# Optimization experiments

Hardware: AMD Instinct MI355X
Metric: run time of the kernel (lower is better)

Reference implementation:

```python
import jax, jax.numpy as jnp
import numpy as np

HEADS = 8
DIM_HEAD = 64
QUERY_DIM = 512
INNER = HEADS * DIM_HEAD
DIAG_OFFSET = 1
T_TEMP = 1.0
NEG_INF = -1e9  # used via -inf below; kept for clarity


def setup_inputs() -> dict:
    key = jax.random.key(0)
    ks = jax.random.split(key, 8)
    b, s, f = 2, 2048, 16
    x = jax.random.normal(ks[0], (b, s, f, QUERY_DIM), dtype=jnp.float32)
    pos_bias = jax.random.normal(ks[1], (HEADS, f, f), dtype=jnp.float32)
    w_scale = 0.02
    Wq = jax.random.normal(ks[2], (QUERY_DIM, INNER), dtype=jnp.float32) * w_scale
    Wk = jax.random.normal(ks[3], (QUERY_DIM, INNER), dtype=jnp.float32) * w_scale
    Wv = jax.random.normal(ks[4], (QUERY_DIM, INNER), dtype=jnp.float32) * w_scale
    Wo = jax.random.normal(ks[5], (INNER, QUERY_DIM), dtype=jnp.float32) * w_scale
    bo = jax.random.normal(ks[6], (QUERY_DIM,), dtype=jnp.float32) * w_scale
    return {"x": x, "pos_bias": pos_bias, "Wq": Wq, "Wk": Wk, "Wv": Wv, "Wo": Wo, "bo": bo}


def reference(x, pos_bias, Wq, Wk, Wv, Wo, bo):
    # x: [b, s, f, c] -- temporal attention over the frame axis f per spatial token
    b, s, f, _ = x.shape
    scale = DIM_HEAD ** -0.5
    q = (x @ Wq).reshape(b, s, f, HEADS, DIM_HEAD)
    k = (x @ Wk).reshape(b, s, f, HEADS, DIM_HEAD)
    v = (x @ Wv).reshape(b, s, f, HEADS, DIM_HEAD)
    # scores over frames: [b, s, h, f_q, f_k]
    w = jnp.einsum('bsihd,bsjhd->bshij', q * scale, k)
    w = w + pos_bias[None, None]  # [h, f, f] relative position bias
    # attend_prev_only causal mask (strict, diag_offset=1)
    causal = jnp.triu(jnp.ones((f, f), dtype=jnp.float32), k=DIAG_OFFSET)
    w = w + jnp.where(causal == 1.0, -jnp.inf, 0.0)
    # faithful to source: subtract row max, then softmax with temperature
    w = w - jax.lax.stop_gradient(jnp.max(w, axis=-1, keepdims=True))
    p = jax.nn.softmax(w.astype(jnp.float32) / T_TEMP, axis=-1).astype(w.dtype)
    out = jnp.einsum('bshij,bsjhd->bsihd', p, v).reshape(b, s, f, INNER)
    return out @ Wo + bo
```

## Files before the change

kernel.cpp:

```cpp
#include <hip/hip_runtime.h>

typedef unsigned short u16;
typedef __attribute__((ext_vector_type(8))) unsigned short u16x8;
typedef __attribute__((ext_vector_type(8))) __bf16 bf16x8;
typedef __attribute__((ext_vector_type(4))) float f32x4;

#define M_ROWS 65536
#define KDIM   512
#define NKT    8

typedef __attribute__((address_space(1))) const void gconst_void;
typedef __attribute__((address_space(3))) void lds_void;

static __device__ __forceinline__ u16 f2bf(float f) {
  unsigned u = __builtin_bit_cast(unsigned, f);
  u += 0x7FFFu + ((u >> 16) & 1u);
  return (u16)(u >> 16);
}

static __device__ __forceinline__ f32x4 mfma_bf16(u16x8 a, u16x8 b, f32x4 c) {
  return __builtin_amdgcn_mfma_f32_16x16x32_bf16(
      __builtin_bit_cast(bf16x8, a), __builtin_bit_cast(bf16x8, b), c, 0, 0, 0);
}

__global__ void conv_x(const float* __restrict__ x, u16* __restrict__ xb) {
  const size_t t = (size_t)blockIdx.x * 256 + threadIdx.x;
  f32x4 a = *(const f32x4*)(x + t * 8);
  f32x4 b = *(const f32x4*)(x + t * 8 + 4);
  u16x8 w;
#pragma unroll
  for (int e = 0; e < 4; ++e) { w[e] = f2bf(a[e]); w[e + 4] = f2bf(b[e]); }
  *(u16x8*)(xb + t * 8) = w;
}

__global__ void convW_qkv_t(const float* __restrict__ Wq, const float* __restrict__ Wk,
                            const float* __restrict__ Wv, u16* __restrict__ Wt) {
  __shared__ float tile[32][33];
  const int bn = blockIdx.x * 32;
  const int bk = blockIdx.y * 32;
  const int tx = threadIdx.x & 31, ty = threadIdx.x >> 5;
  const float* W = (bn < 512) ? Wq : ((bn < 1024) ? Wk : Wv);
  const int coln = bn & 511;
#pragma unroll
  for (int r = 0; r < 32; r += 8)
    tile[ty + r][tx] = W[(size_t)(bk + ty + r) * 512 + coln + tx];
  __syncthreads();
#pragma unroll
  for (int r = 0; r < 32; r += 8)
    Wt[(size_t)(bn + ty + r) * 512 + bk + tx] = f2bf(tile[tx][ty + r]);
}

__global__ void convWo_t(const float* __restrict__ Wo, u16* __restrict__ Wt) {
  __shared__ float tile[32][33];
  const int bn = blockIdx.x * 32;
  const int bk = blockIdx.y * 32;
  const int tx = threadIdx.x & 31, ty = threadIdx.x >> 5;
#pragma unroll
  for (int r = 0; r < 32; r += 8)
    tile[ty + r][tx] = Wo[(size_t)(bk + ty + r) * 512 + bn + tx];
  __syncthreads();
#pragma unroll
  for (int r = 0; r < 32; r += 8)
    Wt[(size_t)(bn + ty + r) * 512 + bk + tx] = f2bf(tile[tx][ty + r]);
}

__global__ __launch_bounds__(512, 2)
void gemm_qkv_attn(const u16* __restrict__ A, const u16* __restrict__ Wt,
                   const float* __restrict__ pos_bias, u16* __restrict__ attnbuf) {
  __shared__ __attribute__((aligned(16))) u16 smem[73728];
  u16* Ab   = smem;
  u16* Bb   = smem + 49152;
  u16* qkvT = smem;
  u16* Pl   = smem + 51200;

  const int tid  = threadIdx.x;
  const int lane = tid & 63;
  const int wid  = tid >> 6;
  const int wm   = wid >> 1;
  const int wn   = wid & 1;
  const int lg   = lane >> 4;
  const int lc   = lane & 15;
  const int srow = lane >> 3;
  const int sg   = (lane & 7) ^ srow;

  const int nwg  = gridDim.x;
  const int cpx  = nwg >> 3;
  const int flat = blockIdx.x;
  const int swz  = (flat & 7) * cpx + (flat >> 3);
  const int mt   = swz >> 3;
  const int h    = swz & 7;
  const int row0 = mt * 256;

  auto stageA = [&](int buf, int unit, int kt) {
    const int rl = unit * 64 + wid * 8;
    const u16* src = A + (size_t)(row0 + rl + srow) * KDIM + kt * 64 + sg * 8;
    __builtin_amdgcn_global_load_lds((gconst_void*)src,
                                     (lds_void*)&Ab[buf * 16384 + rl * 64], 16, 0, 0);
  };
  auto stageB = [&](int buf, int unit, int kt) {
    const int rl = unit * 64 + wid * 8;
    const int grow = unit * 512 + h * 64 + wid * 8 + srow;
    const u16* src = Wt + (size_t)grow * KDIM + kt * 64 + sg * 8;
    __builtin_amdgcn_global_load_lds((gconst_void*)src,
                                     (lds_void*)&Bb[buf * 12288 + rl * 64], 16, 0, 0);
  };

  f32x4 acc[4][6];
#pragma unroll
  for (int mi = 0; mi < 4; ++mi)
#pragma unroll
    for (int ni = 0; ni < 6; ++ni) acc[mi][ni] = (f32x4){0.f, 0.f, 0.f, 0.f};

#pragma unroll
  for (int u = 0; u < 4; ++u) stageA(0, u, 0);
#pragma unroll
  for (int u = 0; u < 3; ++u) stageB(0, u, 0);
#pragma unroll
  for (int u = 0; u < 4; ++u) stageA(1, u, 1);

  for (int t = 0; t < NKT; ++t) {
    const int  ab   = t % 3;
    const int  bb   = t & 1;
    const bool preB = (t + 1) < NKT;
    const bool preA = (t + 2) < NKT;
    const int  ab2  = (t + 2) % 3;

    if (t < NKT - 1) asm volatile("s_waitcnt vmcnt(4)" ::: "memory");
    else             asm volatile("s_waitcnt vmcnt(0)" ::: "memory");
    __builtin_amdgcn_s_barrier();

    if (preB) { stageB(bb ^ 1, 0, t + 1); stageB(bb ^ 1, 1, t + 1); stageB(bb ^ 1, 2, t + 1); }
    if (preA) { stageA(ab2, 0, t + 2); stageA(ab2, 1, t + 2);
                stageA(ab2, 2, t + 2); stageA(ab2, 3, t + 2); }

#pragma unroll
    for (int ks = 0; ks < 2; ++ks) {
      const int gsw = ((ks * 4 + lg) ^ (lc & 7)) << 3;
      u16x8 bfr[6], af[4];
#pragma unroll
      for (int ni = 0; ni < 6; ++ni)
        bfr[ni] = *(const u16x8*)&Bb[bb * 12288 + (wn * 96 + ni * 16 + lc) * 64 + gsw];
#pragma unroll
      for (int i = 0; i < 4; ++i)
        af[i] = *(const u16x8*)&Ab[ab * 16384 + (wm * 64 + i * 16 + lc) * 64 + gsw];
#pragma unroll
      for (int i = 0; i < 4; ++i)
#pragma unroll
        for (int ni = 0; ni < 6; ++ni)
          acc[i][ni] = mfma_bf16(af[i], bfr[ni], acc[i][ni]);
    }
  }
  __syncthreads();

#pragma unroll
  for (int mi = 0; mi < 4; ++mi)
#pragma unroll
    for (int ni = 0; ni < 6; ++ni) {
      const int col = wn * 96 + ni * 16 + lc;
      const int rb  = wm * 64 + mi * 16 + lg * 4;
#pragma unroll
      for (int r = 0; r < 4; ++r)
        qkvT[(rb + r) * 200 + col] = f2bf(acc[mi][ni][r]);
    }
  __syncthreads();

  const float scale = 0.125f;
  const f32x4 zf = {0.f, 0.f, 0.f, 0.f};
#pragma unroll
  for (int tt = 0; tt < 2; ++tt) {
    const int tok = wid * 2 + tt;
    const int rb  = tok * 16;
    const int qb  = (rb + lc) * 200;

    u16x8 aq0 = *(const u16x8*)&qkvT[qb + 0  + lg * 8];
    u16x8 aq1 = *(const u16x8*)&qkvT[qb + 32 + lg * 8];
    u16x8 bk0 = *(const u16x8*)&qkvT[qb + 64 + lg * 8];
    u16x8 bk1 = *(const u16x8*)&qkvT[qb + 96 + lg * 8];
    f32x4 s = mfma_bf16(aq0, bk0, zf);
    s = mfma_bf16(aq1, bk1, s);

    const int pb = wid * 512 + tt * 256;
#pragma unroll
    for (int r = 0; r < 4; ++r) {
      const int i = lg * 4 + r;
      float sv = s[r] * scale + pos_bias[h * 256 + i * 16 + lc];
      if (lc > i) sv = -1e30f;
      float m = sv;
#pragma unroll
      for (int off = 8; off >= 1; off >>= 1) m = fmaxf(m, __shfl_xor(m, off));
      float e = __expf(sv - m);
      float sm = e;
#pragma unroll
      for (int off = 8; off >= 1; off >>= 1) sm += __shfl_xor(sm, off);
      Pl[pb + i * 16 + lc] = f2bf(e / sm);
    }
    asm volatile("s_waitcnt lgkmcnt(0)" ::: "memory");

    u16x8 ap = {0, 0, 0, 0, 0, 0, 0, 0};
    if (lane < 32) ap = *(const u16x8*)&Pl[pb + lc * 16 + lg * 8];

#pragma unroll
    for (int nd = 0; nd < 4; ++nd) {
      u16x8 bv = {0, 0, 0, 0, 0, 0, 0, 0};
      if (lane < 32) {
#pragma unroll
        for (int jj = 0; jj < 8; ++jj) {
          const int j = lg * 8 + jj;
          bv[jj] = qkvT[(rb + j) * 200 + 128 + nd * 16 + lc];
        }
      }
      f32x4 o = mfma_bf16(ap, bv, zf);
#pragma unroll
      for (int r = 0; r < 4; ++r) {
        const int i = lg * 4 + r;
        attnbuf[(size_t)(row0 + rb + i) * 512 + h * 64 + nd * 16 + lc] = f2bf(o[r]);
      }
    }
  }
}

__global__ __launch_bounds__(512, 2)
void gemm_out(const u16* __restrict__ A, const u16* __restrict__ Bt,
              float* __restrict__ C, const float* __restrict__ bias) {
  __shared__ __attribute__((aligned(16))) u16 smem[65536];
  u16* Ab = smem;
  u16* Bb = smem + 49152;

  const int tid  = threadIdx.x;
  const int lane = tid & 63;
  const int wid  = tid >> 6;
  const int wm   = wid >> 1;
  const int wn   = wid & 1;
  const int lg   = lane >> 4;
  const int lc   = lane & 15;
  const int srow = lane >> 3;
  const int sg   = (lane & 7) ^ srow;

  const int nwg  = gridDim.x;
  const int cpx  = nwg >> 3;
  const int flat = blockIdx.x;
  const int swz  = (flat & 7) * cpx + (flat >> 3);
  const int mt   = swz >> 2;
  const int nt   = swz & 3;
  const int row0 = mt * 256, col0 = nt * 128;

  auto stageA = [&](int buf, int unit, int kt) {
    const int rl = unit * 64 + wid * 8;
    const u16* src = A + (size_t)(row0 + rl + srow) * KDIM + kt * 64 + sg * 8;
    __builtin_amdgcn_global_load_lds((gconst_void*)src,
                                     (lds_void*)&Ab[buf * 16384 + rl * 64], 16, 0, 0);
  };
  auto stageB = [&](int buf, int unit, int kt) {
    const int rl = unit * 64 + wid * 8;
    const u16* src = Bt + (size_t)(col0 + rl + srow) * KDIM + kt * 64 + sg * 8;
    __builtin_amdgcn_global_load_lds((gconst_void*)src,
                                     (lds_void*)&Bb[buf * 8192 + rl * 64], 16, 0, 0);
  };

  f32x4 acc[4][4];
#pragma unroll
  for (int mi = 0; mi < 4; ++mi)
#pragma unroll
    for (int ni = 0; ni < 4; ++ni) acc[mi][ni] = (f32x4){0.f, 0.f, 0.f, 0.f};

#pragma unroll
  for (int u = 0; u < 4; ++u) stageA(0, u, 0);
#pragma unroll
  for (int u = 0; u < 2; ++u) stageB(0, u, 0);
#pragma unroll
  for (int u = 0; u < 4; ++u) stageA(1, u, 1);

  for (int t = 0; t < NKT; ++t) {
    const int  ab   = t % 3;
    const int  bb   = t & 1;
    const bool preB = (t + 1) < NKT;
    const bool preA = (t + 2) < NKT;
    const int  ab2  = (t + 2) % 3;

    if (t < NKT - 1) asm volatile("s_waitcnt vmcnt(4)" ::: "memory");
    else             asm volatile("s_waitcnt vmcnt(0)" ::: "memory");
    __builtin_amdgcn_s_barrier();

    if (preB) { stageB(bb ^ 1, 0, t + 1); stageB(bb ^ 1, 1, t + 1); }
    if (preA) { stageA(ab2, 0, t + 2); stageA(ab2, 1, t + 2);
                stageA(ab2, 2, t + 2); stageA(ab2, 3, t + 2); }

#pragma unroll
    for (int ks = 0; ks < 2; ++ks) {
      const int gsw = ((ks * 4 + lg) ^ (lc & 7)) << 3;
      u16x8 bfr[4], af[4];
#pragma unroll
      for (int ni = 0; ni < 4; ++ni)
        bfr[ni] = *(const u16x8*)&Bb[bb * 8192 + (wn * 64 + ni * 16 + lc) * 64 + gsw];
#pragma unroll
      for (int i = 0; i < 4; ++i)
        af[i] = *(const u16x8*)&Ab[ab * 16384 + (wm * 64 + i * 16 + lc) * 64 + gsw];
#pragma unroll
      for (int i = 0; i < 4; ++i)
#pragma unroll
        for (int ni = 0; ni < 4; ++ni)
          acc[i][ni] = mfma_bf16(af[i], bfr[ni], acc[i][ni]);
    }
  }

  const int gmb = row0 + wm * 64;
  const int gnb = col0 + wn * 64;
#pragma unroll
  for (int mi = 0; mi < 4; ++mi)
#pragma unroll
    for (int ni = 0; ni < 4; ++ni) {
      const int gm = gmb + mi * 16 + lg * 4;
      const int gn = gnb + ni * 16 + lc;
      const float bv = bias[gn];
      f32x4 v = acc[mi][ni];
#pragma unroll
      for (int r = 0; r < 4; ++r) C[(size_t)(gm + r) * 512 + gn] = v[r] + bv;
    }
}

extern "C" void kernel_launch(void* const* d_in, const int* in_sizes, int n_in,
                              void* d_out, int out_size, void* d_ws, size_t ws_size,
                              hipStream_t stream) {
  const float* x        = (const float*)d_in[0];
  const float* pos_bias = (const float*)d_in[1];
  const float* Wq       = (const float*)d_in[2];
  const float* Wk       = (const float*)d_in[3];
  const float* Wv       = (const float*)d_in[4];
  const float* Wo       = (const float*)d_in[5];
  const float* bo       = (const float*)d_in[6];
  float* out            = (float*)d_out;

  u16* xb      = (u16*)d_ws;
  u16* attnbuf = xb + (size_t)M_ROWS * 512;
  u16* Wo_t    = attnbuf + (size_t)M_ROWS * 512;
  u16* Wqkv_t  = (u16*)d_out;

  conv_x<<<dim3(M_ROWS * KDIM / (256 * 8)), dim3(256), 0, stream>>>(x, xb);
  convW_qkv_t<<<dim3(48, 16), dim3(256), 0, stream>>>(Wq, Wk, Wv, Wqkv_t);
  gemm_qkv_attn<<<dim3(2048), dim3(512), 0, stream>>>(xb, Wqkv_t, pos_bias, attnbuf);
  convWo_t<<<dim3(16, 16), dim3(256), 0, stream>>>(Wo, Wo_t);
  gemm_out<<<dim3(1024), dim3(512), 0, stream>>>(attnbuf, Wo_t, out, bo);
}
```

Before: 220.6 us.

## Halve QKV-attention tile rows and switch to double-buffered pipeline for higher occupancy

The fused QKV-projection plus attention kernel now handles 128 rows per workgroup instead of 256. The 8 waves are rearranged as 2x4 and each wave keeps 4x3 accumulators. The grid doubles to 4096 blocks, LDS drops to about 80KB, and launch bounds target 4 blocks per CU, all aimed at higher occupancy and better latency hiding. The 3-stage A / 2-stage B prefetch is replaced by a simpler double buffer with a full vmcnt(0) wait and barrier every k-step. This exposes more load latency per block and re-reads the weight tile twice as often across the grid.

```diff
diff --git a/kernel.cpp b/kernel.cpp
--- a/kernel.cpp
+++ b/kernel.cpp
@@ -64,20 +64,20 @@
     Wt[(size_t)(bn + ty + r) * 512 + bk + tx] = f2bf(tile[tx][ty + r]);
 }
 
-__global__ __launch_bounds__(512, 2)
+__global__ __launch_bounds__(512, 4)
 void gemm_qkv_attn(const u16* __restrict__ A, const u16* __restrict__ Wt,
                    const float* __restrict__ pos_bias, u16* __restrict__ attnbuf) {
-  __shared__ __attribute__((aligned(16))) u16 smem[73728];
+  __shared__ __attribute__((aligned(16))) u16 smem[40960];
   u16* Ab   = smem;
-  u16* Bb   = smem + 49152;
+  u16* Bb   = smem + 16384;
   u16* qkvT = smem;
-  u16* Pl   = smem + 51200;
+  u16* Pl   = smem + 25600;
 
   const int tid  = threadIdx.x;
   const int lane = tid & 63;
   const int wid  = tid >> 6;
-  const int wm   = wid >> 1;
-  const int wn   = wid & 1;
+  const int wm   = wid >> 2;
+  const int wn   = wid & 3;
   const int lg   = lane >> 4;
   const int lc   = lane & 15;
   const int srow = lane >> 3;
@@ -89,13 +89,13 @@
   const int swz  = (flat & 7) * cpx + (flat >> 3);
   const int mt   = swz >> 3;
   const int h    = swz & 7;
-  const int row0 = mt * 256;
+  const int row0 = mt * 128;
 
   auto stageA = [&](int buf, int unit, int kt) {
     const int rl = unit * 64 + wid * 8;
     const u16* src = A + (size_t)(row0 + rl + srow) * KDIM + kt * 64 + sg * 8;
     __builtin_amdgcn_global_load_lds((gconst_void*)src,
-                                     (lds_void*)&Ab[buf * 16384 + rl * 64], 16, 0, 0);
+                                     (lds_void*)&Ab[buf * 8192 + rl * 64], 16, 0, 0);
   };
   auto stageB = [&](int buf, int unit, int kt) {
     const int rl = unit * 64 + wid * 8;
@@ -105,58 +105,52 @@
                                      (lds_void*)&Bb[buf * 12288 + rl * 64], 16, 0, 0);
   };
 
-  f32x4 acc[4][6];
+  f32x4 acc[4][3];
 #pragma unroll
   for (int mi = 0; mi < 4; ++mi)
 #pragma unroll
-    for (int ni = 0; ni < 6; ++ni) acc[mi][ni] = (f32x4){0.f, 0.f, 0.f, 0.f};
-
-#pragma unroll
-  for (int u = 0; u < 4; ++u) stageA(0, u, 0);
-#pragma unroll
-  for (int u = 0; u < 3; ++u) stageB(0, u, 0);
-#pragma unroll
-  for (int u = 0; u < 4; ++u) stageA(1, u, 1);
+    for (int ni = 0; ni < 3; ++ni) acc[mi][ni] = (f32x4){0.f, 0.f, 0.f, 0.f};
+
+  stageA(0, 0, 0); stageA(0, 1, 0);
+  stageB(0, 0, 0); stageB(0, 1, 0); stageB(0, 2, 0);
+  asm volatile("s_waitcnt vmcnt(0)" ::: "memory");
+  __builtin_amdgcn_s_barrier();
 
   for (int t = 0; t < NKT; ++t) {
-    const int  ab   = t % 3;
-    const int  bb   = t & 1;
-    const bool preB = (t + 1) < NKT;
-    const bool preA = (t + 2) < NKT;
-    const int  ab2  = (t + 2) % 3;
-
-    if (t < NKT - 1) asm volatile("s_waitcnt vmcnt(4)" ::: "memory");
-    else             asm volatile("s_waitcnt vmcnt(0)" ::: "memory");
-    __builtin_amdgcn_s_barrier();
-
-    if (preB) { stageB(bb ^ 1, 0, t + 1); stageB(bb ^ 1, 1, t + 1); stageB(bb ^ 1, 2, t + 1); }
-    if (preA) { stageA(ab2, 0, t + 2); stageA(ab2, 1, t + 2);
-                stageA(ab2, 2, t + 2); stageA(ab2, 3, t + 2); }
+    const int  c   = t & 1;
+    const bool pre = (t + 1) < NKT;
+
+    if (pre) {
+      stageA(c ^ 1, 0, t + 1); stageA(c ^ 1, 1, t + 1);
+      stageB(c ^ 1, 0, t + 1); stageB(c ^ 1, 1, t + 1); stageB(c ^ 1, 2, t + 1);
+    }
 
 #pragma unroll
     for (int ks = 0; ks < 2; ++ks) {
       const int gsw = ((ks * 4 + lg) ^ (lc & 7)) << 3;
-      u16x8 bfr[6], af[4];
-#pragma unroll
-      for (int ni = 0; ni < 6; ++ni)
-        bfr[ni] = *(const u16x8*)&Bb[bb * 12288 + (wn * 96 + ni * 16 + lc) * 64 + gsw];
+      u16x8 bfr[3], af[4];
+#pragma unroll
+      for (int ni = 0; ni < 3; ++ni)
+        bfr[ni] = *(const u16x8*)&Bb[c * 12288 + (wn * 48 + ni * 16 + lc) * 64 + gsw];
 #pragma unroll
       for (int i = 0; i < 4; ++i)
-        af[i] = *(const u16x8*)&Ab[ab * 16384 + (wm * 64 + i * 16 + lc) * 64 + gsw];
+        af[i] = *(const u16x8*)&Ab[c * 8192 + (wm * 64 + i * 16 + lc) * 64 + gsw];
 #pragma unroll
       for (int i = 0; i < 4; ++i)
 #pragma unroll
-        for (int ni = 0; ni < 6; ++ni)
+        for (int ni = 0; ni < 3; ++ni)
           acc[i][ni] = mfma_bf16(af[i], bfr[ni], acc[i][ni]);
     }
+
+    asm volatile("s_waitcnt vmcnt(0)" ::: "memory");
+    __builtin_amdgcn_s_barrier();
   }
-  __syncthreads();
 
 #pragma unroll
   for (int mi = 0; mi < 4; ++mi)
 #pragma unroll
-    for (int ni = 0; ni < 6; ++ni) {
-      const int col = wn * 96 + ni * 16 + lc;
+    for (int ni = 0; ni < 3; ++ni) {
+      const int col = wn * 48 + ni * 16 + lc;
       const int rb  = wm * 64 + mi * 16 + lg * 4;
 #pragma unroll
       for (int r = 0; r < 4; ++r)
@@ -166,55 +160,51 @@
 
   const float scale = 0.125f;
   const f32x4 zf = {0.f, 0.f, 0.f, 0.f};
-#pragma unroll
-  for (int tt = 0; tt < 2; ++tt) {
-    const int tok = wid * 2 + tt;
-    const int rb  = tok * 16;
-    const int qb  = (rb + lc) * 200;
-
-    u16x8 aq0 = *(const u16x8*)&qkvT[qb + 0  + lg * 8];
-    u16x8 aq1 = *(const u16x8*)&qkvT[qb + 32 + lg * 8];
-    u16x8 bk0 = *(const u16x8*)&qkvT[qb + 64 + lg * 8];
-    u16x8 bk1 = *(const u16x8*)&qkvT[qb + 96 + lg * 8];
-    f32x4 s = mfma_bf16(aq0, bk0, zf);
-    s = mfma_bf16(aq1, bk1, s);
-
-    const int pb = wid * 512 + tt * 256;
+  const int rb = wid * 16;
+  const int qb = (rb + lc) * 200;
+
+  u16x8 aq0 = *(const u16x8*)&qkvT[qb + 0  + lg * 8];
+  u16x8 aq1 = *(const u16x8*)&qkvT[qb + 32 + lg * 8];
+  u16x8 bk0 = *(const u16x8*)&qkvT[qb + 64 + lg * 8];
+  u16x8 bk1 = *(const u16x8*)&qkvT[qb + 96 + lg * 8];
+  f32x4 s = mfma_bf16(aq0, bk0, zf);
+  s = mfma_bf16(aq1, bk1, s);
+
+  const int pb = wid * 256;
+#pragma unroll
+  for (int r = 0; r < 4; ++r) {
+    const int i = lg * 4 + r;
+    float sv = s[r] * scale + pos_bias[h * 256 + i * 16 + lc];
+    if (lc > i) sv = -1e30f;
+    float m = sv;
+#pragma unroll
+    for (int off = 8; off >= 1; off >>= 1) m = fmaxf(m, __shfl_xor(m, off));
+    float e = __expf(sv - m);
+    float sm = e;
+#pragma unroll
+    for (int off = 8; off >= 1; off >>= 1) sm += __shfl_xor(sm, off);
+    Pl[pb + i * 16 + lc] = f2bf(e / sm);
+  }
+  asm volatile("s_waitcnt lgkmcnt(0)" ::: "memory");
+
+  u16x8 ap = {0, 0, 0, 0, 0, 0, 0, 0};
+  if (lane < 32) ap = *(const u16x8*)&Pl[pb + lc * 16 + lg * 8];
+
+#pragma unroll
+  for (int nd = 0; nd < 4; ++nd) {
+    u16x8 bv = {0, 0, 0, 0, 0, 0, 0, 0};
+    if (lane < 32) {
+#pragma unroll
+      for (int jj = 0; jj < 8; ++jj) {
+        const int j = lg * 8 + jj;
+        bv[jj] = qkvT[(rb + j) * 200 + 128 + nd * 16 + lc];
+      }
+    }
+    f32x4 o = mfma_bf16(ap, bv, zf);
 #pragma unroll
     for (int r = 0; r < 4; ++r) {
       const int i = lg * 4 + r;
-      float sv = s[r] * scale + pos_bias[h * 256 + i * 16 + lc];
-      if (lc > i) sv = -1e30f;
-      float m = sv;
-#pragma unroll
-      for (int off = 8; off >= 1; off >>= 1) m = fmaxf(m, __shfl_xor(m, off));
-      float e = __expf(sv - m);
-      float sm = e;
-#pragma unroll
-      for (int off = 8; off >= 1; off >>= 1) sm += __shfl_xor(sm, off);
-      Pl[pb + i * 16 + lc] = f2bf(e / sm);
-    }
-    asm volatile("s_waitcnt lgkmcnt(0)" ::: "memory");
-
-    u16x8 ap = {0, 0, 0, 0, 0, 0, 0, 0};
-    if (lane < 32) ap = *(const u16x8*)&Pl[pb + lc * 16 + lg * 8];
-
-#pragma unroll
-    for (int nd = 0; nd < 4; ++nd) {
-      u16x8 bv = {0, 0, 0, 0, 0, 0, 0, 0};
-      if (lane < 32) {
-#pragma unroll
-        for (int jj = 0; jj < 8; ++jj) {
-          const int j = lg * 8 + jj;
-          bv[jj] = qkvT[(rb + j) * 200 + 128 + nd * 16 + lc];
-        }
-      }
-      f32x4 o = mfma_bf16(ap, bv, zf);
-#pragma unroll
-      for (int r = 0; r < 4; ++r) {
-        const int i = lg * 4 + r;
-        attnbuf[(size_t)(row0 + rb + i) * 512 + h * 64 + nd * 16 + lc] = f2bf(o[r]);
-      }
+      attnbuf[(size_t)(row0 + rb + i) * 512 + h * 64 + nd * 16 + lc] = f2bf(o[r]);
     }
   }
 }
@@ -337,7 +327,7 @@
 
   conv_x<<<dim3(M_ROWS * KDIM / (256 * 8)), dim3(256), 0, stream>>>(x, xb);
   convW_qkv_t<<<dim3(48, 16), dim3(256), 0, stream>>>(Wq, Wk, Wv, Wqkv_t);
-  gemm_qkv_attn<<<dim3(2048), dim3(512), 0, stream>>>(xb, Wqkv_t, pos_bias, attnbuf);
+  gemm_qkv_attn<<<dim3(4096), dim3(512), 0, stream>>>(xb, Wqkv_t, pos_bias, attnbuf);
   convWo_t<<<dim3(16, 16), dim3(256), 0, stream>>>(Wo, Wo_t);
   gemm_out<<<dim3(1024), dim3(512), 0, stream>>>(attnbuf, Wo_t, out, bo);
 }
```

Result: faster. 210.7 us (-4.5%).
